# Optimization experiments

Hardware: AMD Instinct MI355X
Metric: run time of the kernel (lower is better)

Reference implementation:

```python
import jax, jax.numpy as jnp
import numpy as np

VOCAB = 32000
HIDDEN = 512


def setup_inputs() -> dict:
    key = jax.random.key(0)
    k1, k2, k3, k4 = jax.random.split(key, 4)
    B, L = 64, 2048  # batch of trees, leaves per (complete binary) tree
    leaf_ids = jax.random.randint(k1, (B, L), 0, VOCAB)
    emb = jax.random.normal(k2, (VOCAB, HIDDEN), dtype=jnp.float32)
    # nn.Linear(2H, H): weight [H, 2H], bias [H]
    lim = 1.0 / np.sqrt(2 * HIDDEN)
    W = jax.random.uniform(k3, (HIDDEN, 2 * HIDDEN), minval=-lim, maxval=lim, dtype=jnp.float32)
    b = jax.random.uniform(k4, (HIDDEN,), minval=-lim, maxval=lim, dtype=jnp.float32)
    return {"leaf_ids": leaf_ids, "emb": emb, "W": W, "b": b}


def reference(leaf_ids, emb, W, b):
    # Preterminal nodes: embed leaf token then activation (matches original order).
    h = jnp.tanh(emb[leaf_ids])  # [B, L, H]
    B, L, H = h.shape
    n_levels = int(np.log2(L))
    # Bottom-up: each internal node concatenates its two children -> linear -> tanh.
    # All same-depth nodes processed as one batched GEMM.
    for _ in range(n_levels):
        n = h.shape[1]
        pairs = h.reshape(B, n // 2, 2 * H)          # concat(left, right) along feature dim
        h = jnp.tanh(jnp.einsum('bnf,hf->bnh', pairs, W) + b)
    return h  # [B, 1, H] root hidden state per tree
```

## Files before the change

kernel.cpp:

```cpp
#include <hip/hip_runtime.h>
#include <stdint.h>

typedef __attribute__((ext_vector_type(8))) short short8;
typedef __attribute__((ext_vector_type(4))) float floatx4;

__device__ __forceinline__ unsigned short f2bf(float x) {
    unsigned int u = __builtin_bit_cast(unsigned int, x);
    unsigned int r = (u + 0x7FFFu + ((u >> 16) & 1u)) >> 16;
    return (unsigned short)r;
}
__device__ __forceinline__ float bf2f(unsigned short x) {
    unsigned int u = ((unsigned int)x) << 16;
    return __builtin_bit_cast(float, u);
}

__device__ __forceinline__ float fast_tanh(float x) {
    float xc = fminf(fmaxf(x, -10.0f), 10.0f);
    float e  = __expf(2.0f * xc);
    float d  = e + 1.0f;
    float r  = __builtin_amdgcn_rcpf(d);
    r = r * (2.0f - d * r);
    return (e - 1.0f) * r;
}

__global__ void wconv(const float4* __restrict__ W4, ushort4* __restrict__ Wb4) {
    int i = blockIdx.x * 256 + threadIdx.x;
    float4 v = W4[i];
    ushort4 o;
    o.x = f2bf(v.x); o.y = f2bf(v.y); o.z = f2bf(v.z); o.w = f2bf(v.w);
    Wb4[i] = o;
}

__global__ void tconv(const float4* __restrict__ emb4, ushort4* __restrict__ embT4) {
    int i = blockIdx.x * 256 + threadIdx.x;
    float4 v = emb4[i];
    ushort4 o;
    o.x = f2bf(fast_tanh(v.x)); o.y = f2bf(fast_tanh(v.y));
    o.z = f2bf(fast_tanh(v.z)); o.w = f2bf(fast_tanh(v.w));
    embT4[i] = o;
}

#define STAGE_(sA, sB, Ap, Bp, buf, k0)                                         \
    do {                                                                        \
        __builtin_amdgcn_global_load_lds(                                       \
            (const __attribute__((address_space(1))) void*)((Ap) + (k0)),       \
            (__attribute__((address_space(3))) void*)&sA[buf][tid * 8], 16, 0, 0); \
        __builtin_amdgcn_global_load_lds(                                       \
            (const __attribute__((address_space(1))) void*)((Ap) + 64 * 1024 + (k0)), \
            (__attribute__((address_space(3))) void*)&sA[buf][2048 + tid * 8], 16, 0, 0); \
        __builtin_amdgcn_global_load_lds(                                       \
            (const __attribute__((address_space(1))) void*)((Bp) + (k0)),       \
            (__attribute__((address_space(3))) void*)&sB[buf][tid * 8], 16, 0, 0); \
        __builtin_amdgcn_global_load_lds(                                       \
            (const __attribute__((address_space(1))) void*)((Bp) + 64 * 1024 + (k0)), \
            (__attribute__((address_space(3))) void*)&sB[buf][2048 + tid * 8], 16, 0, 0); \
    } while (0)

#define STAGE_PQ(sA, sB, Ap, Bp, buf, k0)                                       \
    do {                                                                        \
        __builtin_amdgcn_global_load_lds(                                       \
            (const __attribute__((address_space(1))) void*)((Ap) + (k0)),       \
            (__attribute__((address_space(3))) void*)&sA[buf][tid * 8], 16, 0, 0); \
        __builtin_amdgcn_global_load_lds(                                       \
            (const __attribute__((address_space(1))) void*)((Ap) + 64 * 512 + (k0)), \
            (__attribute__((address_space(3))) void*)&sA[buf][2048 + tid * 8], 16, 0, 0); \
        __builtin_amdgcn_global_load_lds(                                       \
            (const __attribute__((address_space(1))) void*)((Bp) + (k0)),       \
            (__attribute__((address_space(3))) void*)&sB[buf][tid * 8], 16, 0, 0); \
        __builtin_amdgcn_global_load_lds(                                       \
            (const __attribute__((address_space(1))) void*)((Bp) + 64 * 1024 + (k0)), \
            (__attribute__((address_space(3))) void*)&sB[buf][2048 + tid * 8], 16, 0, 0); \
    } while (0)

#define COMPUTE_(sA, sB, cur)                                                   \
    do {                                                                        \
        short8 a_[4], b_[4];                                                    \
        _Pragma("unroll")                                                       \
        for (int mi = 0; mi < 4; ++mi)                                          \
            a_[mi] = *reinterpret_cast<const short8*>(&sA[cur][(rA + mi * 16) * 32 + kksw]); \
        _Pragma("unroll")                                                       \
        for (int ni = 0; ni < 4; ++ni)                                          \
            b_[ni] = *reinterpret_cast<const short8*>(&sB[cur][(rB + ni * 16) * 32 + kksw]); \
        __builtin_amdgcn_s_setprio(1);                                          \
        _Pragma("unroll")                                                       \
        for (int mi = 0; mi < 4; ++mi)                                          \
            _Pragma("unroll")                                                   \
            for (int ni = 0; ni < 4; ++ni)                                      \
                acc[mi][ni] = __builtin_amdgcn_mfma_f32_16x16x32_bf16(          \
                    a_[mi], b_[ni], acc[mi][ni], 0, 0, 0);                      \
        __builtin_amdgcn_s_setprio(0);                                          \
    } while (0)

#define ITER_S_(STG, sA, sB, cur, stg, tile)                                    \
    do {                                                                        \
        asm volatile("s_barrier" ::: "memory");                                 \
        STG(sA, sB, Ap, Bp, stg, (tile) * 32);                                  \
        asm volatile("s_waitcnt vmcnt(4)" ::: "memory");                        \
        COMPUTE_(sA, sB, cur);                                                  \
    } while (0)

#define ITER_D_(sA, sB, cur)                                                    \
    do {                                                                        \
        asm volatile("s_barrier" ::: "memory");                                 \
        asm volatile("s_waitcnt vmcnt(0)" ::: "memory");                        \
        COMPUTE_(sA, sB, cur);                                                  \
    } while (0)

__global__ __launch_bounds__(256)
void pq_gemm(const ushort* __restrict__ embT, const ushort* __restrict__ Bt,
             ushort* __restrict__ PQ)
{
    const int nb  = gridDim.x;
    int bid = blockIdx.x;
    const int per = nb >> 3;
    const int lin = (bid & 7) * per + (bid >> 3);
    const int table = lin / 1000;
    const int rem   = lin - table * 1000;
    const int mt = rem >> 2, nt = rem & 3;
    const int m0 = mt * 128, n0 = nt * 128;

    __shared__ alignas(16) ushort sA[3][4096];
    __shared__ alignas(16) ushort sB[3][4096];

    const int tid  = threadIdx.x;
    const int lane = tid & 63;
    const int w    = tid >> 6;
    const int wr   = w >> 1, wc = w & 1;

    const int sr    = tid >> 2;
    const int swcol = (((tid & 3) ^ ((tid >> 3) & 3)) << 3);
    const ushort* Ap = embT + (size_t)(m0 + sr) * 512 + swcol;
    const ushort* Bp = Bt + (size_t)(n0 + sr) * 1024 + (table << 9) + swcol;

    const int rA   = wr * 64 + (lane & 15);
    const int rB   = wc * 64 + (lane & 15);
    const int kksw = (((lane >> 4) ^ ((lane >> 1) & 3)) << 3);

    floatx4 acc[4][4] = {};

    STAGE_PQ(sA, sB, Ap, Bp, 0, 0);
    STAGE_PQ(sA, sB, Ap, Bp, 1, 32);
    for (int t = 0; t < 12; t += 3) {
        ITER_S_(STAGE_PQ, sA, sB, 0, 2, t + 2);
        ITER_S_(STAGE_PQ, sA, sB, 1, 0, t + 3);
        ITER_S_(STAGE_PQ, sA, sB, 2, 1, t + 4);
    }
    ITER_S_(STAGE_PQ, sA, sB, 0, 2, 14);
    ITER_S_(STAGE_PQ, sA, sB, 1, 0, 15);
    ITER_D_(sA, sB, 2);
    ITER_D_(sA, sB, 0);

    ushort* outp = PQ + (size_t)table * 16384000;
    const int mrow = (lane >> 4) * 4;
    const int ncol = lane & 15;
    #pragma unroll
    for (int mi = 0; mi < 4; ++mi)
        #pragma unroll
        for (int ni = 0; ni < 4; ++ni) {
            const int n = n0 + wc * 64 + ni * 16 + ncol;
            #pragma unroll
            for (int j = 0; j < 4; ++j) {
                const int m = m0 + wr * 64 + mi * 16 + mrow + j;
                outp[(size_t)m * 512 + n] = f2bf(acc[mi][ni][j]);
            }
        }
}

__global__ void lvl1_add(const int* __restrict__ ids, const ushort* __restrict__ PQ,
                         const float* __restrict__ bias, ushort* __restrict__ h1)
{
    int idx = blockIdx.x * 256 + threadIdx.x;
    int m = idx >> 6;
    int c = (idx & 63) << 3;
    const int il = ids[2 * m], ir = ids[2 * m + 1];
    const short8 p = *reinterpret_cast<const short8*>(PQ + (size_t)il * 512 + c);
    const short8 q = *reinterpret_cast<const short8*>(PQ + 16384000 + (size_t)ir * 512 + c);
    const float4 b0 = *reinterpret_cast<const float4*>(bias + c);
    const float4 b1 = *reinterpret_cast<const float4*>(bias + c + 4);
    short8 o;
    o[0] = (short)f2bf(fast_tanh(bf2f((unsigned short)p[0]) + bf2f((unsigned short)q[0]) + b0.x));
    o[1] = (short)f2bf(fast_tanh(bf2f((unsigned short)p[1]) + bf2f((unsigned short)q[1]) + b0.y));
    o[2] = (short)f2bf(fast_tanh(bf2f((unsigned short)p[2]) + bf2f((unsigned short)q[2]) + b0.z));
    o[3] = (short)f2bf(fast_tanh(bf2f((unsigned short)p[3]) + bf2f((unsigned short)q[3]) + b0.w));
    o[4] = (short)f2bf(fast_tanh(bf2f((unsigned short)p[4]) + bf2f((unsigned short)q[4]) + b1.x));
    o[5] = (short)f2bf(fast_tanh(bf2f((unsigned short)p[5]) + bf2f((unsigned short)q[5]) + b1.y));
    o[6] = (short)f2bf(fast_tanh(bf2f((unsigned short)p[6]) + bf2f((unsigned short)q[6]) + b1.z));
    o[7] = (short)f2bf(fast_tanh(bf2f((unsigned short)p[7]) + bf2f((unsigned short)q[7]) + b1.w));
    *reinterpret_cast<short8*>(h1 + (size_t)idx * 8) = o;
}

__global__ __launch_bounds__(256)
void level_gemm(const ushort* __restrict__ A, const ushort* __restrict__ Bt,
                const float* __restrict__ bias,
                ushort* __restrict__ outb, int M)
{
    const int nb  = gridDim.x;
    int bid = blockIdx.x;
    const int per = nb >> 3;
    const int lin = (bid & 7) * per + (bid >> 3);
    const int mt = lin >> 2, nt = lin & 3;
    const int m0 = mt * 128, n0 = nt * 128;

    __shared__ alignas(16) ushort sA[3][4096];
    __shared__ alignas(16) ushort sB[3][4096];

    const int tid  = threadIdx.x;
    const int lane = tid & 63;
    const int w    = tid >> 6;
    const int wr   = w >> 1, wc = w & 1;

    const int sr    = tid >> 2;
    const int swcol = (((tid & 3) ^ ((tid >> 3) & 3)) << 3);
    const ushort* Ap = A  + (size_t)(m0 + sr) * 1024 + swcol;
    const ushort* Bp = Bt + (size_t)(n0 + sr) * 1024 + swcol;

    const int rA   = wr * 64 + (lane & 15);
    const int rB   = wc * 64 + (lane & 15);
    const int kksw = (((lane >> 4) ^ ((lane >> 1) & 3)) << 3);

    floatx4 acc[4][4] = {};

    STAGE_(sA, sB, Ap, Bp, 0, 0);
    STAGE_(sA, sB, Ap, Bp, 1, 32);
    for (int t = 0; t < 30; t += 3) {
        ITER_S_(STAGE_, sA, sB, 0, 2, t + 2);
        ITER_S_(STAGE_, sA, sB, 1, 0, t + 3);
        ITER_S_(STAGE_, sA, sB, 2, 1, t + 4);
    }
    ITER_D_(sA, sB, 0);
    ITER_D_(sA, sB, 1);

    const int mrow = (lane >> 4) * 4;
    const int ncol = lane & 15;
    #pragma unroll
    for (int mi = 0; mi < 4; ++mi)
        #pragma unroll
        for (int ni = 0; ni < 4; ++ni) {
            const int n = n0 + wc * 64 + ni * 16 + ncol;
            const float bb = bias[n];
            #pragma unroll
            for (int j = 0; j < 4; ++j) {
                const int m = m0 + wr * 64 + mi * 16 + mrow + j;
                float v = fast_tanh(acc[mi][ni][j] + bb);
                outb[(size_t)m * 512 + n] = f2bf(v);
            }
        }
}

__global__ __launch_bounds__(256)
void small_gemm(const ushort* __restrict__ A, const ushort* __restrict__ Bt,
                const float* __restrict__ bias,
                ushort* __restrict__ outb, float* __restrict__ outf, int last)
{
    __shared__ alignas(16) ushort sA[3][4096];
    __shared__ alignas(16) ushort sB[3][4096];

    const int tid  = threadIdx.x;
    const int lane = tid & 63;
    const int w    = tid >> 6;
    const int l15  = lane & 15;
    const int lh   = lane >> 4;
    const int mt   = blockIdx.x >> 3, nt = blockIdx.x & 7;
    const int m0   = mt * 64, n0 = nt * 64;

    const int r0 = tid >> 3;
    const int s0 = tid & 7;
    const int swz = ((s0 ^ (r0 & 7)) << 3);
    const ushort* Ap = A  + (size_t)(m0 + r0) * 1024 + swz;
    const ushort* Bp = Bt + (size_t)(n0 + r0) * 1024 + swz;

#define STG6(buf, k0)                                                           \
    do {                                                                        \
        __builtin_amdgcn_global_load_lds(                                       \
            (const __attribute__((address_space(1))) void*)(Ap + (k0)),         \
            (__attribute__((address_space(3))) void*)&sA[buf][tid * 8], 16, 0, 0); \
        __builtin_amdgcn_global_load_lds(                                       \
            (const __attribute__((address_space(1))) void*)(Ap + 32 * 1024 + (k0)), \
            (__attribute__((address_space(3))) void*)&sA[buf][2048 + tid * 8], 16, 0, 0); \
        __builtin_amdgcn_global_load_lds(                                       \
            (const __attribute__((address_space(1))) void*)(Bp + (k0)),         \
            (__attribute__((address_space(3))) void*)&sB[buf][tid * 8], 16, 0, 0); \
        __builtin_amdgcn_global_load_lds(                                       \
            (const __attribute__((address_space(1))) void*)(Bp + 32 * 1024 + (k0)), \
            (__attribute__((address_space(3))) void*)&sB[buf][2048 + tid * 8], 16, 0, 0); \
    } while (0)

    const int rb = w * 16 + l15;
    floatx4 acc[4] = {};

#define CMP6(buf)                                                               \
    do {                                                                        \
        _Pragma("unroll")                                                       \
        for (int ks = 0; ks < 2; ++ks) {                                        \
            const int kq = ks * 4 + lh;                                         \
            const short8 b_ = *reinterpret_cast<const short8*>(                 \
                &sB[buf][rb * 64 + ((kq ^ (rb & 7)) << 3)]);                    \
            __builtin_amdgcn_s_setprio(1);                                      \
            _Pragma("unroll")                                                   \
            for (int mi = 0; mi < 4; ++mi) {                                    \
                const int ra = mi * 16 + l15;                                   \
                const short8 a_ = *reinterpret_cast<const short8*>(             \
                    &sA[buf][ra * 64 + ((kq ^ (l15 & 7)) << 3)]);               \
                acc[mi] = __builtin_amdgcn_mfma_f32_16x16x32_bf16(              \
                    a_, b_, acc[mi], 0, 0, 0);                                  \
            }                                                                   \
            __builtin_amdgcn_s_setprio(0);                                      \
        }                                                                       \
    } while (0)

    STG6(0, 0);
    STG6(1, 64);
    for (int t3 = 0; t3 < 12; t3 += 3) {
        asm volatile("s_barrier" ::: "memory");
        STG6(2, (t3 + 2) * 64);
        asm volatile("s_waitcnt vmcnt(4)" ::: "memory");
        CMP6(0);
        asm volatile("s_barrier" ::: "memory");
        STG6(0, (t3 + 3) * 64);
        asm volatile("s_waitcnt vmcnt(4)" ::: "memory");
        CMP6(1);
        asm volatile("s_barrier" ::: "memory");
        STG6(1, (t3 + 4) * 64);
        asm volatile("s_waitcnt vmcnt(4)" ::: "memory");
        CMP6(2);
    }
    asm volatile("s_barrier" ::: "memory");
    STG6(2, 14 * 64);
    asm volatile("s_waitcnt vmcnt(8)" ::: "memory");
    CMP6(0);
    asm volatile("s_barrier" ::: "memory");
    STG6(0, 15 * 64);
    asm volatile("s_waitcnt vmcnt(8)" ::: "memory");
    CMP6(1);
    asm volatile("s_barrier" ::: "memory");
    asm volatile("s_waitcnt vmcnt(4)" ::: "memory");
    CMP6(2);
    asm volatile("s_barrier" ::: "memory");
    asm volatile("s_waitcnt vmcnt(0)" ::: "memory");
    CMP6(0);
#undef CMP6
#undef STG6

    const int n  = n0 + w * 16 + l15;
    const float bb = bias[n];
    #pragma unroll
    for (int mi = 0; mi < 4; ++mi) {
        #pragma unroll
        for (int j = 0; j < 4; ++j) {
            const int m = m0 + mi * 16 + lh * 4 + j;
            float v = fast_tanh(acc[mi][j] + bb);
            if (last) outf[(size_t)m * 512 + n] = v;
            else      outb[(size_t)m * 512 + n] = f2bf(v);
        }
    }
}

extern "C" void kernel_launch(void* const* d_in, const int* in_sizes, int n_in,
                              void* d_out, int out_size, void* d_ws, size_t ws_size,
                              hipStream_t stream) {
    const int*   ids  = (const int*)d_in[0];
    const float* emb  = (const float*)d_in[1];
    const float* W    = (const float*)d_in[2];
    const float* bias = (const float*)d_in[3];
    float* out = (float*)d_out;

    unsigned short* Wb   = (unsigned short*)d_ws;
    unsigned short* embT = Wb + 524288;
    unsigned short* PQ   = embT + 16384000;
    unsigned short* hB   = PQ + 32768000;
    unsigned short* hA   = hB + 33554432;

    wconv<<<512, 256, 0, stream>>>((const float4*)W, (ushort4*)Wb);
    tconv<<<16000, 256, 0, stream>>>((const float4*)emb, (ushort4*)embT);

    pq_gemm<<<2000, 256, 0, stream>>>(embT, Wb, PQ);
    lvl1_add<<<16384, 256, 0, stream>>>(ids, PQ, bias, hB);

    int M = 32768;
    for (int l = 2; l <= 4; ++l) {
        const unsigned short* in = (l & 1) ? hA : hB;
        unsigned short*       ob = (l & 1) ? hB : hA;
        level_gemm<<<(M / 128) * 4, 256, 0, stream>>>(in, Wb, bias, ob, M);
        M >>= 1;
    }
    for (int l = 5; l <= 11; ++l) {
        const unsigned short* in = (l & 1) ? hA : hB;
        unsigned short*       ob = (l & 1) ? hB : hA;
        small_gemm<<<(M / 64) * 8, 256, 0, stream>>>(in, Wb, bias, ob, out,
                                                     l == 11 ? 1 : 0);
        M >>= 1;
    }
}
```

Baseline: 274.2 us.

## Replace 128x128 GEMMs with 256x256-tile 512-thread double-buffered kernel

The PQ table GEMM and the large-level GEMMs now share one templated kernel. It uses 256x256 output tiles, 8 waves per block each computing 128x64, and double-buffered LDS staging in place of triple buffering. Larger tiles raise arithmetic intensity and halve the redundant reloads of A and W per output. In exchange the block count drops (500 blocks for PQ, fewer for the levels), LDS per block grows to 64KB, and there are 128 accumulator registers per thread, which risks low occupancy and tail effects on 256 CUs.

```diff
diff --git a/kernel.cpp b/kernel.cpp
--- a/kernel.cpp
+++ b/kernel.cpp
@@ -38,132 +38,6 @@
     o.x = f2bf(fast_tanh(v.x)); o.y = f2bf(fast_tanh(v.y));
     o.z = f2bf(fast_tanh(v.z)); o.w = f2bf(fast_tanh(v.w));
     embT4[i] = o;
-}
-
-#define STAGE_(sA, sB, Ap, Bp, buf, k0)                                         \
-    do {                                                                        \
-        __builtin_amdgcn_global_load_lds(                                       \
-            (const __attribute__((address_space(1))) void*)((Ap) + (k0)),       \
-            (__attribute__((address_space(3))) void*)&sA[buf][tid * 8], 16, 0, 0); \
-        __builtin_amdgcn_global_load_lds(                                       \
-            (const __attribute__((address_space(1))) void*)((Ap) + 64 * 1024 + (k0)), \
-            (__attribute__((address_space(3))) void*)&sA[buf][2048 + tid * 8], 16, 0, 0); \
-        __builtin_amdgcn_global_load_lds(                                       \
-            (const __attribute__((address_space(1))) void*)((Bp) + (k0)),       \
-            (__attribute__((address_space(3))) void*)&sB[buf][tid * 8], 16, 0, 0); \
-        __builtin_amdgcn_global_load_lds(                                       \
-            (const __attribute__((address_space(1))) void*)((Bp) + 64 * 1024 + (k0)), \
-            (__attribute__((address_space(3))) void*)&sB[buf][2048 + tid * 8], 16, 0, 0); \
-    } while (0)
-
-#define STAGE_PQ(sA, sB, Ap, Bp, buf, k0)                                       \
-    do {                                                                        \
-        __builtin_amdgcn_global_load_lds(                                       \
-            (const __attribute__((address_space(1))) void*)((Ap) + (k0)),       \
-            (__attribute__((address_space(3))) void*)&sA[buf][tid * 8], 16, 0, 0); \
-        __builtin_amdgcn_global_load_lds(                                       \
-            (const __attribute__((address_space(1))) void*)((Ap) + 64 * 512 + (k0)), \
-            (__attribute__((address_space(3))) void*)&sA[buf][2048 + tid * 8], 16, 0, 0); \
-        __builtin_amdgcn_global_load_lds(                                       \
-            (const __attribute__((address_space(1))) void*)((Bp) + (k0)),       \
-            (__attribute__((address_space(3))) void*)&sB[buf][tid * 8], 16, 0, 0); \
-        __builtin_amdgcn_global_load_lds(                                       \
-            (const __attribute__((address_space(1))) void*)((Bp) + 64 * 1024 + (k0)), \
-            (__attribute__((address_space(3))) void*)&sB[buf][2048 + tid * 8], 16, 0, 0); \
-    } while (0)
-
-#define COMPUTE_(sA, sB, cur)                                                   \
-    do {                                                                        \
-        short8 a_[4], b_[4];                                                    \
-        _Pragma("unroll")                                                       \
-        for (int mi = 0; mi < 4; ++mi)                                          \
-            a_[mi] = *reinterpret_cast<const short8*>(&sA[cur][(rA + mi * 16) * 32 + kksw]); \
-        _Pragma("unroll")                                                       \
-        for (int ni = 0; ni < 4; ++ni)                                          \
-            b_[ni] = *reinterpret_cast<const short8*>(&sB[cur][(rB + ni * 16) * 32 + kksw]); \
-        __builtin_amdgcn_s_setprio(1);                                          \
-        _Pragma("unroll")                                                       \
-        for (int mi = 0; mi < 4; ++mi)                                          \
-            _Pragma("unroll")                                                   \
-            for (int ni = 0; ni < 4; ++ni)                                      \
-                acc[mi][ni] = __builtin_amdgcn_mfma_f32_16x16x32_bf16(          \
-                    a_[mi], b_[ni], acc[mi][ni], 0, 0, 0);                      \
-        __builtin_amdgcn_s_setprio(0);                                          \
-    } while (0)
-
-#define ITER_S_(STG, sA, sB, cur, stg, tile)                                    \
-    do {                                                                        \
-        asm volatile("s_barrier" ::: "memory");                                 \
-        STG(sA, sB, Ap, Bp, stg, (tile) * 32);                                  \
-        asm volatile("s_waitcnt vmcnt(4)" ::: "memory");                        \
-        COMPUTE_(sA, sB, cur);                                                  \
-    } while (0)
-
-#define ITER_D_(sA, sB, cur)                                                    \
-    do {                                                                        \
-        asm volatile("s_barrier" ::: "memory");                                 \
-        asm volatile("s_waitcnt vmcnt(0)" ::: "memory");                        \
-        COMPUTE_(sA, sB, cur);                                                  \
-    } while (0)
-
-__global__ __launch_bounds__(256)
-void pq_gemm(const ushort* __restrict__ embT, const ushort* __restrict__ Bt,
-             ushort* __restrict__ PQ)
-{
-    const int nb  = gridDim.x;
-    int bid = blockIdx.x;
-    const int per = nb >> 3;
-    const int lin = (bid & 7) * per + (bid >> 3);
-    const int table = lin / 1000;
-    const int rem   = lin - table * 1000;
-    const int mt = rem >> 2, nt = rem & 3;
-    const int m0 = mt * 128, n0 = nt * 128;
-
-    __shared__ alignas(16) ushort sA[3][4096];
-    __shared__ alignas(16) ushort sB[3][4096];
-
-    const int tid  = threadIdx.x;
-    const int lane = tid & 63;
-    const int w    = tid >> 6;
-    const int wr   = w >> 1, wc = w & 1;
-
-    const int sr    = tid >> 2;
-    const int swcol = (((tid & 3) ^ ((tid >> 3) & 3)) << 3);
-    const ushort* Ap = embT + (size_t)(m0 + sr) * 512 + swcol;
-    const ushort* Bp = Bt + (size_t)(n0 + sr) * 1024 + (table << 9) + swcol;
-
-    const int rA   = wr * 64 + (lane & 15);
-    const int rB   = wc * 64 + (lane & 15);
-    const int kksw = (((lane >> 4) ^ ((lane >> 1) & 3)) << 3);
-
-    floatx4 acc[4][4] = {};
-
-    STAGE_PQ(sA, sB, Ap, Bp, 0, 0);
-    STAGE_PQ(sA, sB, Ap, Bp, 1, 32);
-    for (int t = 0; t < 12; t += 3) {
-        ITER_S_(STAGE_PQ, sA, sB, 0, 2, t + 2);
-        ITER_S_(STAGE_PQ, sA, sB, 1, 0, t + 3);
-        ITER_S_(STAGE_PQ, sA, sB, 2, 1, t + 4);
-    }
-    ITER_S_(STAGE_PQ, sA, sB, 0, 2, 14);
-    ITER_S_(STAGE_PQ, sA, sB, 1, 0, 15);
-    ITER_D_(sA, sB, 2);
-    ITER_D_(sA, sB, 0);
-
-    ushort* outp = PQ + (size_t)table * 16384000;
-    const int mrow = (lane >> 4) * 4;
-    const int ncol = lane & 15;
-    #pragma unroll
-    for (int mi = 0; mi < 4; ++mi)
-        #pragma unroll
-        for (int ni = 0; ni < 4; ++ni) {
-            const int n = n0 + wc * 64 + ni * 16 + ncol;
-            #pragma unroll
-            for (int j = 0; j < 4; ++j) {
-                const int m = m0 + wr * 64 + mi * 16 + mrow + j;
-                outp[(size_t)m * 512 + n] = f2bf(acc[mi][ni][j]);
-            }
-        }
 }
 
 __global__ void lvl1_add(const int* __restrict__ ids, const ushort* __restrict__ PQ,
@@ -189,62 +63,120 @@
     *reinterpret_cast<short8*>(h1 + (size_t)idx * 8) = o;
 }
 
-__global__ __launch_bounds__(256)
-void level_gemm(const ushort* __restrict__ A, const ushort* __restrict__ Bt,
-                const float* __restrict__ bias,
-                ushort* __restrict__ outb, int M)
+#define STG256(buf, k0)                                                         \
+    do {                                                                        \
+        __builtin_amdgcn_global_load_lds(                                       \
+            (const __attribute__((address_space(1))) void*)(Ap + (k0)),         \
+            (__attribute__((address_space(3))) void*)&sA[buf][tid * 8], 16, 0, 0); \
+        __builtin_amdgcn_global_load_lds(                                       \
+            (const __attribute__((address_space(1))) void*)(Ap + 128 * ASTR + (k0)), \
+            (__attribute__((address_space(3))) void*)&sA[buf][4096 + tid * 8], 16, 0, 0); \
+        __builtin_amdgcn_global_load_lds(                                       \
+            (const __attribute__((address_space(1))) void*)(Bp + (k0)),         \
+            (__attribute__((address_space(3))) void*)&sB[buf][tid * 8], 16, 0, 0); \
+        __builtin_amdgcn_global_load_lds(                                       \
+            (const __attribute__((address_space(1))) void*)(Bp + 128 * 1024 + (k0)), \
+            (__attribute__((address_space(3))) void*)&sB[buf][4096 + tid * 8], 16, 0, 0); \
+    } while (0)
+
+#define CMP256(buf)                                                             \
+    do {                                                                        \
+        short8 a_[8], b_[4];                                                    \
+        _Pragma("unroll")                                                       \
+        for (int mi = 0; mi < 8; ++mi)                                          \
+            a_[mi] = *reinterpret_cast<const short8*>(&sA[buf][(rA + mi * 16) * 32 + kksw]); \
+        _Pragma("unroll")                                                       \
+        for (int ni = 0; ni < 4; ++ni)                                          \
+            b_[ni] = *reinterpret_cast<const short8*>(&sB[buf][(rB + ni * 16) * 32 + kksw]); \
+        __builtin_amdgcn_s_setprio(1);                                          \
+        _Pragma("unroll")                                                       \
+        for (int mi = 0; mi < 8; ++mi)                                          \
+            _Pragma("unroll")                                                   \
+            for (int ni = 0; ni < 4; ++ni)                                      \
+                acc[mi][ni] = __builtin_amdgcn_mfma_f32_16x16x32_bf16(          \
+                    a_[mi], b_[ni], acc[mi][ni], 0, 0, 0);                      \
+        __builtin_amdgcn_s_setprio(0);                                          \
+    } while (0)
+
+template<int ASTR, int NT, int MODE>
+__global__ __launch_bounds__(512)
+void gemm256(const ushort* __restrict__ A, const ushort* __restrict__ Bt,
+             const float* __restrict__ bias, ushort* __restrict__ outb)
 {
-    const int nb  = gridDim.x;
-    int bid = blockIdx.x;
-    const int per = nb >> 3;
-    const int lin = (bid & 7) * per + (bid >> 3);
-    const int mt = lin >> 2, nt = lin & 3;
-    const int m0 = mt * 128, n0 = nt * 128;
-
-    __shared__ alignas(16) ushort sA[3][4096];
-    __shared__ alignas(16) ushort sB[3][4096];
+    __shared__ alignas(16) ushort sA[2][8192];
+    __shared__ alignas(16) ushort sB[2][8192];
 
     const int tid  = threadIdx.x;
     const int lane = tid & 63;
     const int w    = tid >> 6;
-    const int wr   = w >> 1, wc = w & 1;
+    const int wr   = w >> 2, wc = w & 3;
+
+    int mt, ntile, koff = 0;
+    size_t obase = 0;
+    if constexpr (MODE == 0) {
+        const int nb  = gridDim.x;
+        const int per = nb >> 3;
+        const int lin = (blockIdx.x & 7) * per + (blockIdx.x >> 3);
+        mt = lin >> 1; ntile = lin & 1;
+    } else {
+        int bid = blockIdx.x;
+        const int table = (bid >= 250) ? 1 : 0;
+        const int rem = bid - table * 250;
+        mt = rem >> 1; ntile = rem & 1;
+        koff  = table << 9;
+        obase = (size_t)table * 16384000;
+    }
+    const int m0 = mt * 256, n0 = ntile * 256;
 
     const int sr    = tid >> 2;
     const int swcol = (((tid & 3) ^ ((tid >> 3) & 3)) << 3);
-    const ushort* Ap = A  + (size_t)(m0 + sr) * 1024 + swcol;
-    const ushort* Bp = Bt + (size_t)(n0 + sr) * 1024 + swcol;
-
-    const int rA   = wr * 64 + (lane & 15);
-    const int rB   = wc * 64 + (lane & 15);
+    const ushort* Ap = A  + (size_t)(m0 + sr) * ASTR + swcol;
+    const ushort* Bp = Bt + (size_t)(n0 + sr) * 1024 + koff + swcol;
+
+    const int rA   = wr * 128 + (lane & 15);
+    const int rB   = wc * 64  + (lane & 15);
     const int kksw = (((lane >> 4) ^ ((lane >> 1) & 3)) << 3);
 
-    floatx4 acc[4][4] = {};
-
-    STAGE_(sA, sB, Ap, Bp, 0, 0);
-    STAGE_(sA, sB, Ap, Bp, 1, 32);
-    for (int t = 0; t < 30; t += 3) {
-        ITER_S_(STAGE_, sA, sB, 0, 2, t + 2);
-        ITER_S_(STAGE_, sA, sB, 1, 0, t + 3);
-        ITER_S_(STAGE_, sA, sB, 2, 1, t + 4);
-    }
-    ITER_D_(sA, sB, 0);
-    ITER_D_(sA, sB, 1);
+    floatx4 acc[8][4] = {};
+
+    STG256(0, 0);
+    for (int t = 0; t + 2 < NT; t += 2) {
+        asm volatile("s_barrier" ::: "memory");
+        STG256(1, (t + 1) * 32);
+        asm volatile("s_waitcnt vmcnt(4)" ::: "memory");
+        CMP256(0);
+        asm volatile("s_barrier" ::: "memory");
+        STG256(0, (t + 2) * 32);
+        asm volatile("s_waitcnt vmcnt(4)" ::: "memory");
+        CMP256(1);
+    }
+    asm volatile("s_barrier" ::: "memory");
+    STG256(1, (NT - 1) * 32);
+    asm volatile("s_waitcnt vmcnt(4)" ::: "memory");
+    CMP256(0);
+    asm volatile("s_barrier" ::: "memory");
+    asm volatile("s_waitcnt vmcnt(0)" ::: "memory");
+    CMP256(1);
 
     const int mrow = (lane >> 4) * 4;
     const int ncol = lane & 15;
     #pragma unroll
-    for (int mi = 0; mi < 4; ++mi)
+    for (int mi = 0; mi < 8; ++mi) {
         #pragma unroll
         for (int ni = 0; ni < 4; ++ni) {
             const int n = n0 + wc * 64 + ni * 16 + ncol;
-            const float bb = bias[n];
             #pragma unroll
             for (int j = 0; j < 4; ++j) {
-                const int m = m0 + wr * 64 + mi * 16 + mrow + j;
-                float v = fast_tanh(acc[mi][ni][j] + bb);
-                outb[(size_t)m * 512 + n] = f2bf(v);
+                const int m = m0 + wr * 128 + mi * 16 + mrow + j;
+                if constexpr (MODE == 0) {
+                    float v = fast_tanh(acc[mi][ni][j] + bias[n]);
+                    outb[(size_t)m * 512 + n] = f2bf(v);
+                } else {
+                    outb[obase + (size_t)m * 512 + n] = f2bf(acc[mi][ni][j]);
+                }
             }
         }
+    }
 }
 
 __global__ __launch_bounds__(256)
@@ -373,14 +305,14 @@
     wconv<<<512, 256, 0, stream>>>((const float4*)W, (ushort4*)Wb);
     tconv<<<16000, 256, 0, stream>>>((const float4*)emb, (ushort4*)embT);
 
-    pq_gemm<<<2000, 256, 0, stream>>>(embT, Wb, PQ);
+    gemm256<512, 16, 1><<<500, 512, 0, stream>>>(embT, Wb, bias, PQ);
     lvl1_add<<<16384, 256, 0, stream>>>(ids, PQ, bias, hB);
 
     int M = 32768;
     for (int l = 2; l <= 4; ++l) {
         const unsigned short* in = (l & 1) ? hA : hB;
         unsigned short*       ob = (l & 1) ? hB : hA;
-        level_gemm<<<(M / 128) * 4, 256, 0, stream>>>(in, Wb, bias, ob, M);
+        gemm256<1024, 32, 0><<<(M / 256) * 2, 512, 0, stream>>>(in, Wb, bias, ob);
         M >>= 1;
     }
     for (int l = 5; l <= 11; ++l) {
```

Result: slower. 285.3 us (+4.1%).
